# Kernel tuning notes

Hardware: AMD Instinct MI355X
Metric: run time of the kernel (lower is better)

## Reference

```python
import jax, jax.numpy as jnp
import numpy as np

N = 100000      # nodes
E = 1600000     # edges (before self-loops)
F_IN = 128      # dataset.num_features
H1 = 128        # hidden_channels/2
H2 = 256        # hidden_channels
C = 40          # dataset.num_classes
EPS = 1e-5      # BatchNorm eps
NEG_SLOPE = 0.2 # GATConv leaky_relu slope


def setup_inputs() -> dict:
    key = jax.random.key(0)
    ks = jax.random.split(key, 12)
    p = lambda k, shape: jax.random.normal(k, shape, jnp.float32) * 0.1
    x = jax.random.normal(ks[0], (N, F_IN), jnp.float32)
    edge_index = jax.random.randint(ks[1], (2, E), 0, N, dtype=jnp.int64)
    return dict(
        x=x, edge_index=edge_index,
        w1=p(ks[2], (F_IN, H1)), as1=p(ks[3], (H1,)), ad1=p(ks[4], (H1,)), b1=jnp.zeros(H1, jnp.float32),
        g1=jnp.ones(H1, jnp.float32), be1=jnp.zeros(H1, jnp.float32), rm1=jnp.zeros(H1, jnp.float32), rv1=jnp.ones(H1, jnp.float32),
        w2=p(ks[5], (H1, H2)), as2=p(ks[6], (H2,)), ad2=p(ks[7], (H2,)), b2=jnp.zeros(H2, jnp.float32),
        g2=jnp.ones(H2, jnp.float32), be2=jnp.zeros(H2, jnp.float32), rm2=jnp.zeros(H2, jnp.float32), rv2=jnp.ones(H2, jnp.float32),
        w3=p(ks[8], (H2, C)), as3=p(ks[9], (C,)), ad3=p(ks[10], (C,)), b3=jnp.zeros(C, jnp.float32),
    )


def gat_conv(x, src, dst, W, a_src, a_dst, b):
    """PyG GATConv (heads=1, add_self_loops already applied to src/dst)."""
    h = x @ W                                  # [N, F_out]
    alpha_src = h @ a_src                      # [N]
    alpha_dst = h @ a_dst                      # [N]
    logits = jax.nn.leaky_relu(alpha_src[src] + alpha_dst[dst], NEG_SLOPE)  # [E']
    # segment softmax over incoming edges of each dst node
    m = jax.ops.segment_max(logits, dst, num_segments=N)
    e = jnp.exp(logits - m[dst])
    denom = jax.ops.segment_sum(e, dst, num_segments=N)
    alpha = e / denom[dst]                     # [E']
    out = jax.ops.segment_sum(h[src] * alpha[:, None], dst, num_segments=N)
    return out + b


def bn_eval(x, gamma, beta, mean, var):
    return (x - mean) * jax.lax.rsqrt(var + EPS) * gamma + beta


def reference(x, edge_index,
              w1, as1, ad1, b1, g1, be1, rm1, rv1,
              w2, as2, ad2, b2, g2, be2, rm2, rv2,
              w3, as3, ad3, b3):
    # add self-loops once (PyG GATConv default add_self_loops=True)
    loop = jnp.arange(N, dtype=edge_index.dtype)
    src = jnp.concatenate([edge_index[0], loop])
    dst = jnp.concatenate([edge_index[1], loop])
    # eval mode: dropout is identity, BN uses running stats
    h = gat_conv(x, src, dst, w1, as1, ad1, b1)
    h = jnp.tanh(bn_eval(h, g1, be1, rm1, rv1))
    h = gat_conv(h, src, dst, w2, as2, ad2, b2)
    h = jnp.tanh(bn_eval(h, g2, be2, rm2, rv2))
    return gat_conv(h, src, dst, w3, as3, ad3, b3)
```

## Files before the change

kernel.cpp:

```cpp
#include <hip/hip_runtime.h>
#include <hip/hip_bf16.h>
#include <cstddef>

#define N_NODES 100000
#define E_EDGES 1600000
#define TOT_EDGES (E_EDGES + N_NODES)
#define NEG_SLOPE 0.2f
#define BN_EPS 1e-5f
#define NBKT ((N_NODES + 255) / 256)
#define NBA 512

typedef __attribute__((ext_vector_type(8))) short short8;
typedef __attribute__((ext_vector_type(4))) float f32x4;
typedef __attribute__((ext_vector_type(2))) float f32x2;
typedef __attribute__((ext_vector_type(4))) int int32x4;
typedef __attribute__((ext_vector_type(2))) int int32x2;

#if defined(__has_builtin)
#if __has_builtin(__builtin_amdgcn_make_buffer_rsrc) && __has_builtin(__builtin_amdgcn_raw_buffer_load_b128)
#define HAVE_BUFRSRC 1
#endif
#if __has_builtin(__builtin_amdgcn_make_buffer_rsrc) && __has_builtin(__builtin_amdgcn_raw_buffer_load_b64)
#define HAVE_BUF64 1
#endif
#endif

__device__ __forceinline__ unsigned short f2bf(float f) {
    union { float f; unsigned u; } c; c.f = f;
    unsigned u = c.u;
    u += 0x7fffu + ((u >> 16) & 1u);
    return (unsigned short)(u >> 16);
}
__device__ __forceinline__ float bf2f(unsigned short h) {
    union { unsigned u; float f; } c; c.u = ((unsigned)h) << 16;
    return c.f;
}
__device__ __forceinline__ unsigned short f2h(float f) {
    union { _Float16 h; unsigned short u; } c; c.h = (_Float16)f; return c.u;
}
__device__ __forceinline__ float lrelu(float t) {
    return (t > 0.f) ? t : NEG_SLOPE * t;
}
__device__ __forceinline__ float tanh_fast(float x) {
    float e = __expf(2.f * x);
    return 1.f - 2.f / (e + 1.f);
}
__device__ __forceinline__ unsigned short pk_fp8(float a, float b) {
    unsigned v;
    asm volatile("v_cvt_pk_fp8_f32 %0, %1, %2" : "=v"(v) : "v"(a), "v"(b));
    return (unsigned short)v;
}
__device__ __forceinline__ f32x2 unpk_fp8(unsigned u) {
    f32x2 r;
    asm volatile("v_cvt_pk_f32_fp8 %0, %1" : "=v"(r) : "v"(u));
    return r;
}

__device__ __forceinline__ float wave_sum63(float x) {
    x += __int_as_float(__builtin_amdgcn_update_dpp(0, __float_as_int(x), 0x111, 0xf, 0xf, true));
    x += __int_as_float(__builtin_amdgcn_update_dpp(0, __float_as_int(x), 0x112, 0xf, 0xf, true));
    x += __int_as_float(__builtin_amdgcn_update_dpp(0, __float_as_int(x), 0x114, 0xf, 0xf, true));
    x += __int_as_float(__builtin_amdgcn_update_dpp(0, __float_as_int(x), 0x118, 0xf, 0xf, true));
    x += __int_as_float(__builtin_amdgcn_update_dpp(0, __float_as_int(x), 0x142, 0xf, 0xf, true));
    x += __int_as_float(__builtin_amdgcn_update_dpp(0, __float_as_int(x), 0x143, 0xf, 0xf, true));
    return x;
}
__device__ __forceinline__ float wave_sum_bcast(float x) {
    return __int_as_float(__builtin_amdgcn_readlane(__float_as_int(wave_sum63(x)), 63));
}


__global__ __launch_bounds__(256) void csr_hist(const int* __restrict__ ei,
                                                int* __restrict__ bh) {
    __shared__ int h[NBKT];
    int t = threadIdx.x;
    for (int b = t; b < NBKT; b += 256) h[b] = 0;
    __syncthreads();
    int idx = blockIdx.x * 256 + t;
    const int stride = NBA * 256;
    for (int e = idx; e < TOT_EDGES; e += stride) {
        int d = (e < E_EDGES) ? ei[E_EDGES + e] : (e - E_EDGES);
        atomicAdd(&h[((unsigned)d) >> 8], 1);
    }
    __syncthreads();
    for (int b = t; b < NBKT; b += 256) bh[blockIdx.x * NBKT + b] = h[b];
}

__global__ __launch_bounds__(512) void csr_scan_blocks(int* __restrict__ bh,
                                                       int* __restrict__ totals) {
    __shared__ int s[NBA];
    int t = threadIdx.x, bin = blockIdx.x;
    int v = bh[t * NBKT + bin];
    s[t] = v;
    __syncthreads();
    for (int off = 1; off < NBA; off <<= 1) {
        int y = (t >= off) ? s[t - off] : 0;
        __syncthreads();
        s[t] += y;
        __syncthreads();
    }
    bh[t * NBKT + bin] = s[t] - v;
    if (t == NBA - 1) totals[bin] = s[t];
}

__global__ __launch_bounds__(512) void csr_scan_buckets(const int* __restrict__ totals,
                                                        int* __restrict__ starts) {
    __shared__ int s[512];
    int t = threadIdx.x;
    int v = (t < NBKT) ? totals[t] : 0;
    s[t] = v;
    __syncthreads();
    for (int off = 1; off < 512; off <<= 1) {
        int y = (t >= off) ? s[t - off] : 0;
        __syncthreads();
        s[t] += y;
        __syncthreads();
    }
    if (t < NBKT) starts[t] = s[t] - v;
    if (t == 0) starts[NBKT] = TOT_EDGES;
}

__global__ __launch_bounds__(256) void csr_scatter(const int* __restrict__ ei,
                                                   const int* __restrict__ bh,
                                                   const int* __restrict__ starts,
                                                   int* __restrict__ pairs) {
    __shared__ int wp[NBKT];
    int t = threadIdx.x;
    for (int b = t; b < NBKT; b += 256)
        wp[b] = starts[b] + bh[blockIdx.x * NBKT + b];
    __syncthreads();
    int idx = blockIdx.x * 256 + t;
    const int stride = NBA * 256;
    for (int e = idx; e < TOT_EDGES; e += stride) {
        int s, d;
        if (e < E_EDGES) { s = ei[e]; d = ei[E_EDGES + e]; }
        else             { s = e - E_EDGES; d = s; }
        int pos = atomicAdd(&wp[((unsigned)d) >> 8], 1);
        pairs[pos] = s | ((d & 255) << 20);
    }
}

__global__ __launch_bounds__(256) void csr_build(const int* __restrict__ pairs,
                                                 const int* __restrict__ starts,
                                                 int* __restrict__ row_ptr,
                                                 int* __restrict__ src_sorted) {
    __shared__ int nh[256];
    __shared__ int sc[256];
    __shared__ int wp[256];
    int k = blockIdx.x, t = threadIdx.x;
    int bs = starts[k], be = starts[k + 1];
    nh[t] = 0;
    __syncthreads();
    for (int i = bs + t; i < be; i += 256)
        atomicAdd(&nh[((unsigned)pairs[i]) >> 20], 1);
    __syncthreads();
    int v = nh[t];
    sc[t] = v;
    __syncthreads();
    for (int off = 1; off < 256; off <<= 1) {
        int y = (t >= off) ? sc[t - off] : 0;
        __syncthreads();
        sc[t] += y;
        __syncthreads();
    }
    int excl = sc[t] - v;
    int node = k * 256 + t;
    if (node <= N_NODES) row_ptr[node] = bs + excl;
    wp[t] = bs + excl;
    __syncthreads();
    for (int i = bs + t; i < be; i += 256) {
        unsigned p = (unsigned)pairs[i];
        int pos = atomicAdd(&wp[p >> 20], 1);
        src_sorted[pos] = (int)(p & 0xFFFFFu);
    }
}

__global__ __launch_bounds__(256) void wprep_all(
    const float* __restrict__ w1, const float* __restrict__ w2, const float* __restrict__ w3,
    const float* __restrict__ as1, const float* __restrict__ ad1,
    const float* __restrict__ as2, const float* __restrict__ ad2,
    const float* __restrict__ as3, const float* __restrict__ ad3,
    unsigned short* __restrict__ w1th, unsigned short* __restrict__ w1tl,
    unsigned short* __restrict__ w2th, unsigned short* __restrict__ w2tl,
    unsigned short* __restrict__ w3th, unsigned short* __restrict__ w3tl,
    unsigned short* __restrict__ ab1h, unsigned short* __restrict__ ab1l,
    unsigned short* __restrict__ ab3h, unsigned short* __restrict__ ab3l,
    float* __restrict__ ws2f, float* __restrict__ wd2f) {
    const int T1 = 128 * 128, T2 = 256 * 128, T3 = 48 * 256;
    const int W = T1 + T2 + T3;
    int idx = blockIdx.x * 256 + threadIdx.x;
    if (idx < W) {
        float v; unsigned short* th; unsigned short* tl; int o;
        if (idx < T1) {
            int n = idx / 128, k = idx % 128;
            v = w1[k * 128 + n]; th = w1th; tl = w1tl; o = idx;
        } else if (idx < T1 + T2) {
            int i = idx - T1; int n = i / 128, k = i % 128;
            v = w2[k * 256 + n]; th = w2th; tl = w2tl; o = i;
        } else {
            int i = idx - T1 - T2; int n = i / 256, k = i % 256;
            v = (n < 40) ? w3[k * 40 + n] : 0.f; th = w3th; tl = w3tl; o = i;
        }
        unsigned short h = f2bf(v);
        th[o] = h;
        tl[o] = f2bf(v - bf2f(h));
        return;
    }
    int j = idx - W;
    if (j < 2048) {
        int r = j / 128, k = j % 128;
        float v = 0.f;
        if (r < 2) {
            const float* a = r ? ad1 : as1;
            const float* wr = w1 + (size_t)k * 128;
            for (int n = 0; n < 128; n++) v += wr[n] * a[n];
        }
        unsigned short h = f2bf(v);
        ab1h[j] = h; ab1l[j] = f2bf(v - bf2f(h));
    } else if (j < 2048 + 4096) {
        int i = j - 2048; int r = i / 256, k = i % 256;
        float v = 0.f;
        if (r < 2) {
            const float* a = r ? ad3 : as3;
            const float* wr = w3 + (size_t)k * 40;
            for (int n = 0; n < 40; n++) v += wr[n] * a[n];
        }
        unsigned short h = f2bf(v);
        ab3h[i] = h; ab3l[i] = f2bf(v - bf2f(h));
    } else if (j < 2048 + 4096 + 256) {
        int i = j - 2048 - 4096; int r = i / 128, k = i % 128;
        const float* a = r ? ad2 : as2;
        const float* wr = w2 + (size_t)k * 256;
        float v = 0.f;
        for (int n = 0; n < 256; n++) v += wr[n] * a[n];
        if (r == 0) ws2f[k] = v; else wd2f[k] = v;
    }
}

template<int K, int NTILES, int MWAVES, int NWAVES, int NACT, bool ASPLIT, bool ALPHA, bool BNT, bool CFRAG, bool CHALF, bool AF32>
__global__ __launch_bounds__(256) void mfma_gemm(
    const unsigned short* __restrict__ Ahi, const unsigned short* __restrict__ Alo,
    const unsigned short* __restrict__ BThi, const unsigned short* __restrict__ BTlo,
    const unsigned short* __restrict__ ABh, const unsigned short* __restrict__ ABl,
    unsigned short* __restrict__ Chi, int ldc,
    const float* __restrict__ bias, const float* __restrict__ gamma,
    const float* __restrict__ beta, const float* __restrict__ rmean,
    const float* __restrict__ rvar,
    float* __restrict__ asrc, float* __restrict__ adst, int M)
{
    int lane = threadIdx.x & 63;
    int wave = threadIdx.x >> 6;
    int quad = lane >> 4;
    int l16  = lane & 15;
    long mbase = (long)blockIdx.x * (64 * MWAVES) + (long)(wave / NWAVES) * 64;
    int n0 = ((wave % NWAVES) + blockIdx.y * NWAVES) * (NTILES * 16);
    bool aw = ((wave % NWAVES) == 0) && (blockIdx.y == 0);
    const size_t CSTRIDE = (size_t)M * 32;

    size_t roff[4];
#pragma unroll
    for (int i = 0; i < 4; i++) {
        long r = mbase + i * 16 + l16;
        if (r > M - 1) r = M - 1;
        roff[i] = AF32 ? ((size_t)r * K + (size_t)(quad * 8))
                       : ((size_t)r * 32 + (size_t)(quad * 8));
    }
    const unsigned short* bh[NTILES]; const unsigned short* bl[NTILES];
#pragma unroll
    for (int j = 0; j < NTILES; j++) {
        long n = n0 + j * 16 + l16;
        bh[j] = BThi + n * K; bl[j] = BTlo + n * K;
    }
    const unsigned short* bah = nullptr; const unsigned short* bal = nullptr;
    if constexpr (ALPHA) { bah = ABh + (size_t)l16 * K; bal = ABl + (size_t)l16 * K; }
    const int ko = quad * 8;

    f32x4 acc[4][NTILES];
    f32x4 acca[4];
#pragma unroll
    for (int i = 0; i < 4; i++) {
        acca[i] = (f32x4){0.f, 0.f, 0.f, 0.f};
#pragma unroll
        for (int j = 0; j < NTILES; j++)
            acc[i][j] = (f32x4){0.f, 0.f, 0.f, 0.f};
    }

    for (int kc = 0; kc < K / 32; kc++) {
        const int k0 = kc * 32;
        short8 vah[4], vall[4], vbh[NTILES], vbl[NTILES];
#pragma unroll
        for (int i = 0; i < 4; i++) {
            if constexpr (AF32) {
                const float* xf = (const float*)Ahi;
                const float* pa = xf + roff[i] + kc * 32;
                f32x4 va = *(const f32x4*)pa;
                f32x4 vb = *(const f32x4*)(pa + 4);
#pragma unroll
                for (int q = 0; q < 8; q++) {
                    float v = (q < 4) ? va[q] : vb[q - 4];
                    unsigned short h = f2bf(v);
                    vah[i][q] = (short)h;
                    vall[i][q] = (short)f2bf(v - bf2f(h));
                }
            } else {
                const unsigned short* Ah = Ahi + (size_t)kc * CSTRIDE;
                vah[i] = *(const short8*)(Ah + roff[i]);
                if constexpr (ASPLIT) {
                    const unsigned short* Al = Alo + (size_t)kc * CSTRIDE;
                    vall[i] = *(const short8*)(Al + roff[i]);
                }
            }
        }
#pragma unroll
        for (int j = 0; j < NTILES; j++) {
            vbh[j] = *(const short8*)(bh[j] + k0 + ko);
            vbl[j] = *(const short8*)(bl[j] + k0 + ko);
        }
#pragma unroll
        for (int i = 0; i < 4; i++)
#pragma unroll
            for (int j = 0; j < NTILES; j++) {
                acc[i][j] = __builtin_amdgcn_mfma_f32_16x16x32_bf16(vah[i], vbh[j], acc[i][j], 0, 0, 0);
                acc[i][j] = __builtin_amdgcn_mfma_f32_16x16x32_bf16(vah[i], vbl[j], acc[i][j], 0, 0, 0);
                if constexpr (ASPLIT)
                    acc[i][j] = __builtin_amdgcn_mfma_f32_16x16x32_bf16(vall[i], vbh[j], acc[i][j], 0, 0, 0);
            }
        if constexpr (ALPHA) {
            if (aw) {
                short8 vbah = *(const short8*)(bah + k0 + ko);
                short8 vbal = *(const short8*)(bal + k0 + ko);
#pragma unroll
                for (int i = 0; i < 4; i++) {
                    acca[i] = __builtin_amdgcn_mfma_f32_16x16x32_bf16(vah[i], vbah, acca[i], 0, 0, 0);
                    acca[i] = __builtin_amdgcn_mfma_f32_16x16x32_bf16(vah[i], vbal, acca[i], 0, 0, 0);
                    if constexpr (ASPLIT)
                        acca[i] = __builtin_amdgcn_mfma_f32_16x16x32_bf16(vall[i], vbah, acca[i], 0, 0, 0);
                }
            }
        }
    }

#pragma unroll
    for (int i = 0; i < 4; i++)
#pragma unroll
        for (int j = 0; j < NTILES; j++) {
            int col = n0 + j * 16 + l16;
            float bb = 0.f, rs = 1.f, gg = 1.f, bt = 0.f, rm = 0.f;
            if constexpr (BNT) {
                bb = bias[col]; gg = gamma[col]; bt = beta[col];
                rm = rmean[col]; rs = rsqrtf(rvar[col] + BN_EPS);
            }
#pragma unroll
            for (int r = 0; r < 4; r++) {
                long row = mbase + i * 16 + quad * 4 + r;
                if (row < M && col < NACT) {
                    float v = acc[i][j][r];
                    if constexpr (BNT) v = tanh_fast((v + bb - rm) * rs * gg + bt);
                    if constexpr (CFRAG) {
                        Chi[(size_t)(col >> 5) * CSTRIDE + (size_t)row * 32 + (col & 31)] = f2bf(v);
                    } else {
                        Chi[row * ldc + col] = CHALF ? f2h(v) : f2bf(v);
                    }
                }
            }
        }
    if constexpr (ALPHA) {
        if (aw) {
#pragma unroll
            for (int i = 0; i < 4; i++)
#pragma unroll
                for (int r = 0; r < 4; r++) {
                    long row = mbase + i * 16 + quad * 4 + r;
                    if (row < M) {
                        float v = acca[i][r];
                        if (l16 == 0) asrc[row] = v;
                        else if (l16 == 1) adst[row] = v;
                    }
                }
        }
    }
}

__global__ __launch_bounds__(512) void gemm23_fused(
    const unsigned short* __restrict__ Ahi,
    const unsigned short* __restrict__ B2h, const unsigned short* __restrict__ B2l,
    const float* __restrict__ bias, const float* __restrict__ gamma,
    const float* __restrict__ beta, const float* __restrict__ rmean,
    const float* __restrict__ rvar,
    const unsigned short* __restrict__ B3h, const unsigned short* __restrict__ B3l,
    const unsigned short* __restrict__ AB3h, const unsigned short* __restrict__ AB3l,
    unsigned short* __restrict__ h3,
    float* __restrict__ asrc, float* __restrict__ adst, int M)
{
    constexpr int LW = 40;
    __shared__ unsigned short o2l[8 * 64 * LW];

    int lane = threadIdx.x & 63;
    int wave = threadIdx.x >> 6;
    int quad = lane >> 4;
    int l16  = lane & 15;
    long mbase = (long)blockIdx.x * 64;
    const size_t CSTRIDE = (size_t)M * 32;
    const int ko = quad * 8;

    size_t roff[4];
#pragma unroll
    for (int i = 0; i < 4; i++) {
        long r = mbase + i * 16 + l16;
        if (r > M - 1) r = M - 1;
        roff[i] = (size_t)r * 32 + (size_t)ko;
    }
    int n0 = wave * 32;
    const unsigned short* bh[2]; const unsigned short* bl[2];
#pragma unroll
    for (int j = 0; j < 2; j++) {
        long n = n0 + j * 16 + l16;
        bh[j] = B2h + n * 128; bl[j] = B2l + n * 128;
    }

    f32x4 acc[4][2];
#pragma unroll
    for (int i = 0; i < 4; i++)
#pragma unroll
        for (int j = 0; j < 2; j++)
            acc[i][j] = (f32x4){0.f, 0.f, 0.f, 0.f};

#pragma unroll
    for (int kc = 0; kc < 4; kc++) {
        const int k0 = kc * 32;
        const unsigned short* Ah = Ahi + (size_t)kc * CSTRIDE;
        short8 vah[4], vbh[2], vbl[2];
#pragma unroll
        for (int i = 0; i < 4; i++) vah[i] = *(const short8*)(Ah + roff[i]);
#pragma unroll
        for (int j = 0; j < 2; j++) {
            vbh[j] = *(const short8*)(bh[j] + k0 + ko);
            vbl[j] = *(const short8*)(bl[j] + k0 + ko);
        }
#pragma unroll
        for (int i = 0; i < 4; i++)
#pragma unroll
            for (int j = 0; j < 2; j++) {
                acc[i][j] = __builtin_amdgcn_mfma_f32_16x16x32_bf16(vah[i], vbh[j], acc[i][j], 0, 0, 0);
                acc[i][j] = __builtin_amdgcn_mfma_f32_16x16x32_bf16(vah[i], vbl[j], acc[i][j], 0, 0, 0);
            }
    }

#pragma unroll
    for (int j = 0; j < 2; j++) {
        int col = n0 + j * 16 + l16;
        float bb = bias[col], gg = gamma[col], bt = beta[col];
        float rm = rmean[col], rs = rsqrtf(rvar[col] + BN_EPS);
        int cbase = (col >> 5) * 64 * LW + (col & 31);
#pragma unroll
        for (int i = 0; i < 4; i++)
#pragma unroll
            for (int r = 0; r < 4; r++) {
                int li = i * 16 + quad * 4 + r;
                float v = tanh_fast((acc[i][j][r] + bb - rm) * rs * gg + bt);
                o2l[cbase + li * LW] = f2bf(v);
            }
    }
    __syncthreads();

    int rh   = wave >> 2;
    int task = wave & 3;
    int lrow0 = rh * 32 + l16;
    int lrow1 = rh * 32 + 16 + l16;

    const unsigned short* p3h;
    const unsigned short* p3l;
    if (task < 3) {
        p3h = B3h + (size_t)(task * 16 + l16) * 256;
        p3l = B3l + (size_t)(task * 16 + l16) * 256;
    } else {
        p3h = AB3h + (size_t)l16 * 256;
        p3l = AB3l + (size_t)l16 * 256;
    }

    f32x4 a3[2];
    a3[0] = (f32x4){0.f, 0.f, 0.f, 0.f};
    a3[1] = (f32x4){0.f, 0.f, 0.f, 0.f};

#pragma unroll 2
    for (int kc = 0; kc < 8; kc++) {
        const int k0 = kc * 32;
        short8 a0 = *(const short8*)(o2l + (kc * 64 + lrow0) * LW + ko);
        short8 a1 = *(const short8*)(o2l + (kc * 64 + lrow1) * LW + ko);
        short8 vh = *(const short8*)(p3h + k0 + ko);
        short8 vl = *(const short8*)(p3l + k0 + ko);
        a3[0] = __builtin_amdgcn_mfma_f32_16x16x32_bf16(a0, vh, a3[0], 0, 0, 0);
        a3[0] = __builtin_amdgcn_mfma_f32_16x16x32_bf16(a0, vl, a3[0], 0, 0, 0);
        a3[1] = __builtin_amdgcn_mfma_f32_16x16x32_bf16(a1, vh, a3[1], 0, 0, 0);
        a3[1] = __builtin_amdgcn_mfma_f32_16x16x32_bf16(a1, vl, a3[1], 0, 0, 0);
    }

    if (task < 3) {
        int col = task * 16 + l16;
#pragma unroll
        for (int i = 0; i < 2; i++)
#pragma unroll
            for (int r = 0; r < 4; r++) {
                long row = mbase + rh * 32 + i * 16 + quad * 4 + r;
                if (row < M) h3[(size_t)row * 64 + col] = f2h(a3[i][r]);
            }
    } else {
#pragma unroll
        for (int i = 0; i < 2; i++)
#pragma unroll
            for (int r = 0; r < 4; r++) {
                long row = mbase + rh * 32 + i * 16 + quad * 4 + r;
                if (row < M) {
                    if (l16 == 0) asrc[row] = a3[i][r];
                    else if (l16 == 1) adst[row] = a3[i][r];
                }
            }
    }
}

template<int MODE>
__global__ __launch_bounds__(256) void gat_agg_wide(
    const unsigned short* __restrict__ hsrc,
    const float* __restrict__ asrc, const float* __restrict__ adst,
    const int* __restrict__ row_ptr, const int* __restrict__ src_sorted,
    const float* __restrict__ bias, const float* __restrict__ gamma,
    const float* __restrict__ beta, const float* __restrict__ rmean,
    const float* __restrict__ rvar,
    const float* __restrict__ wsn, const float* __restrict__ wdn,
    unsigned short* __restrict__ ohi,
    float* __restrict__ outf,
    float* __restrict__ asrc_n, float* __restrict__ adst_n)
{
    constexpr int SH  = (MODE == 0) ? 8 : 7;
    constexpr int BPL = (MODE == 0) ? 16 : 8;
    constexpr int NF  = (MODE == 2) ? 4 : 8;

    __shared__ __align__(16) float2 esw[4][64];
    __shared__ __align__(16) float red[4][4][132];

    int wave = threadIdx.x >> 6;
    int lane = threadIdx.x & 63;
    int node = blockIdx.x * 4 + wave;
    if (node >= N_NODES) return;

    int start = row_ptr[node];
    int end = row_ptr[node + 1];
    int deg = end - start;
    float ad = adst[node];
    int sub = lane >> 4;
    int foff = (lane & 15) * BPL;
    int tpos = (lane & 3) * 16 + (lane >> 2);

#if defined(HAVE_BUFRSRC) && defined(HAVE_BUF64)
    auto rsrc = __builtin_amdgcn_make_buffer_rsrc((void*)hsrc, (short)0,
                                                  N_NODES << SH, 0x00020000);
#endif

    float acc[NF];
#pragma unroll
    for (int i = 0; i < NF; i++) acc[i] = 0.f;

    auto ld = [&](int vo) {
        if constexpr (MODE == 0) {
#if defined(HAVE_BUFRSRC) && defined(HAVE_BUF64)
            return __builtin_amdgcn_raw_buffer_load_b128(rsrc, vo, 0, 0);
#else
            return *reinterpret_cast<const int32x4*>(
                reinterpret_cast<const char*>(hsrc) + (unsigned)vo);
#endif
        } else {
#if defined(HAVE_BUFRSRC) && defined(HAVE_BUF64)
            return __builtin_amdgcn_raw_buffer_load_b64(rsrc, vo, 0, 0);
#else
            return *reinterpret_cast<const int32x2*>(
                reinterpret_cast<const char*>(hsrc) + (unsigned)vo);
#endif
        }
    };
    auto fmaN = [&](auto u, float ww) {
        if constexpr (MODE == 0) {
            union { decltype(u) v; unsigned w[4]; } c; c.v = u;
#pragma unroll
            for (int i = 0; i < 4; i++) {
                union { unsigned u; _Float16 h[2]; } t; t.u = c.w[i];
                acc[2 * i]     += ww * (float)t.h[0];
                acc[2 * i + 1] += ww * (float)t.h[1];
            }
        } else if constexpr (MODE == 1) {
            union { decltype(u) v; unsigned w[2]; } c; c.v = u;
#pragma unroll
            for (int i = 0; i < 2; i++) {
                f32x2 lo = unpk_fp8(c.w[i]);
                f32x2 hi = unpk_fp8(c.w[i] >> 16);
                acc[4 * i]     += ww * lo.x;
                acc[4 * i + 1] += ww * lo.y;
                acc[4 * i + 2] += ww * hi.x;
                acc[4 * i + 3] += ww * hi.y;
            }
        } else {
            union { decltype(u) v; unsigned w[2]; } c; c.v = u;
#pragma unroll
            for (int i = 0; i < 2; i++) {
                union { unsigned u; _Float16 h[2]; } t; t.u = c.w[i];
                acc[2 * i]     += ww * (float)t.h[0];
                acc[2 * i + 1] += ww * (float)t.h[1];
            }
        }
    };
    auto gather = [&](int nst) {
        const float2* ep = &esw[wave][sub * 16];
#pragma unroll
        for (int b = 0; b < 4; b++) {
            int s0 = b * 4;
            if (s0 < nst) {
                f32x4 p01 = *(const f32x4*)(ep + s0);
                f32x4 p23 = *(const f32x4*)(ep + s0 + 2);
                bool g1 = s0 + 1 < nst, g2 = s0 + 2 < nst, g3 = s0 + 3 < nst;
                auto u0 = ld(__float_as_int(p01.x) + foff);
                decltype(u0) u1, u2, u3;
                if (g1) u1 = ld(__float_as_int(p01.z) + foff);
                if (g2) u2 = ld(__float_as_int(p23.x) + foff);
                if (g3) u3 = ld(__float_as_int(p23.z) + foff);
                fmaN(u0, p01.y);
                if (g1) fmaN(u1, p01.w);
                if (g2) fmaN(u2, p23.y);
                if (g3) fmaN(u3, p23.w);
            }
        }
    };

    if (deg <= 64) {
        int e = start + lane;
        int s = 0; float w = 0.f;
        if (e < end) { s = src_sorted[e]; w = __expf(lrelu(asrc[s] + ad)); }
        float dsum = wave_sum_bcast(w);
        esw[wave][tpos] = make_float2(__int_as_float(s << SH), w * (1.0f / dsum));
        gather((deg + 3) >> 2);
    } else {
        float part = 0.f;
        for (int cs = start; cs < end; cs += 64) {
            int e = cs + lane;
            if (e < end) part += __expf(lrelu(asrc[src_sorted[e]] + ad));
        }
        float inv = 1.0f / wave_sum_bcast(part);
        for (int cs = start; cs < end; cs += 64) {
            int e = cs + lane;
            int s = 0; float w = 0.f;
            if (e < end) { s = src_sorted[e]; w = __expf(lrelu(asrc[s] + ad)) * inv; }
            esw[wave][tpos] = make_float2(__int_as_float(s << SH), w);
            gather((min(64, end - cs) + 3) >> 2);
        }
    }

    if constexpr (MODE == 2) {
        *reinterpret_cast<f32x4*>(&red[wave][sub][(lane & 15) * 4]) =
            (f32x4){acc[0], acc[1], acc[2], acc[3]};
        float t = 0.f;
#pragma unroll
        for (int g = 0; g < 4; g++) t += red[wave][g][lane];
        if (lane < 40) outf[(size_t)node * 40 + lane] = t + bias[lane];
    } else {
        f32x4* dst = reinterpret_cast<f32x4*>(&red[wave][sub][(lane & 15) * 8]);
        dst[0] = (f32x4){acc[0], acc[1], acc[2], acc[3]};
        dst[1] = (f32x4){acc[4], acc[5], acc[6], acc[7]};
        f32x2 tsum = (f32x2){0.f, 0.f};
#pragma unroll
        for (int g = 0; g < 4; g++)
            tsum += *reinterpret_cast<const f32x2*>(&red[wave][g][lane * 2]);

        if constexpr (MODE == 0) {
            float vals[2];
#pragma unroll
            for (int v = 0; v < 2; v++) {
                int f = lane * 2 + v;
                float val = tsum[v] + bias[f];
                float rs = rsqrtf(rvar[f] + BN_EPS);
                vals[v] = tanh_fast((val - rmean[f]) * rs * gamma[f] + beta[f]);
            }
            ohi[(size_t)node * 64 + lane] = pk_fp8(vals[0], vals[1]);
            float ps = vals[0] * wsn[lane * 2] + vals[1] * wsn[lane * 2 + 1];
            float pd = vals[0] * wdn[lane * 2] + vals[1] * wdn[lane * 2 + 1];
            ps = wave_sum63(ps);
            pd = wave_sum63(pd);
            if (lane == 63) { asrc_n[node] = ps; adst_n[node] = pd; }
        } else {
            const size_t CSTRIDE = (size_t)N_NODES * 32;
            unsigned w0 = (unsigned)f2bf(tsum[0]) | ((unsigned)f2bf(tsum[1]) << 16);
            size_t a = (size_t)(lane >> 4) * CSTRIDE + (size_t)node * 32 + ((lane * 2) & 31);
            *reinterpret_cast<unsigned*>(ohi + a) = w0;
        }
    }
}


static inline size_t align256(size_t x) { return (x + 255) & ~(size_t)255; }

extern "C" void kernel_launch(void* const* d_in, const int* in_sizes, int n_in,
                              void* d_out, int out_size, void* d_ws, size_t ws_size,
                              hipStream_t stream) {
    const float* x   = (const float*)d_in[0];
    const int* ei    = (const int*)d_in[1];
    const float* w1  = (const float*)d_in[2];
    const float* as1 = (const float*)d_in[3];
    const float* ad1 = (const float*)d_in[4];
    const float* b1  = (const float*)d_in[5];
    const float* g1  = (const float*)d_in[6];
    const float* be1 = (const float*)d_in[7];
    const float* rm1 = (const float*)d_in[8];
    const float* rv1 = (const float*)d_in[9];
    const float* w2  = (const float*)d_in[10];
    const float* as2 = (const float*)d_in[11];
    const float* ad2 = (const float*)d_in[12];
    const float* b2  = (const float*)d_in[13];
    const float* g2  = (const float*)d_in[14];
    const float* be2 = (const float*)d_in[15];
    const float* rm2 = (const float*)d_in[16];
    const float* rv2 = (const float*)d_in[17];
    const float* w3  = (const float*)d_in[18];
    const float* as3 = (const float*)d_in[19];
    const float* ad3 = (const float*)d_in[20];
    const float* b3  = (const float*)d_in[21];
    float* out = (float*)d_out;

    const size_t P128 = align256((size_t)N_NODES * 128 * 2);
    const size_t P256 = align256((size_t)N_NODES * 256 * 2);

    char* p = (char*)d_ws;
    char* regA = p; p += P256;
    char* regB = p; p += P256;
    unsigned short* o1p  = (unsigned short*)regA;
    unsigned short* h3h  = (unsigned short*)regA;
    unsigned short* h1h  = (unsigned short*)regB;
    unsigned short* g2hi = (unsigned short*)regB;
    int* pairs  = (int*)regB;
    int* bhist  = (int*)(regB + align256((size_t)TOT_EDGES * 4));
    int* totals = (int*)((char*)bhist + align256((size_t)NBA * NBKT * 4));
    int* starts = (int*)((char*)totals + align256((size_t)NBKT * 4));

    float* asrcA = (float*)p; p += align256((size_t)N_NODES * 4);
    float* adstA = (float*)p; p += align256((size_t)N_NODES * 4);
    float* asrcB = (float*)p; p += align256((size_t)N_NODES * 4);
    float* adstB = (float*)p; p += align256((size_t)N_NODES * 4);
    int* row_ptr   = (int*)p; p += align256((size_t)(N_NODES + 1) * 4);
    int* src_sorted = (int*)p; p += align256((size_t)TOT_EDGES * 4);
    unsigned short* w1th = (unsigned short*)p; p += align256(128 * 128 * 2);
    unsigned short* w1tl = (unsigned short*)p; p += align256(128 * 128 * 2);
    unsigned short* w2th = (unsigned short*)p; p += align256(256 * 128 * 2);
    unsigned short* w2tl = (unsigned short*)p; p += align256(256 * 128 * 2);
    unsigned short* w3th = (unsigned short*)p; p += align256(48 * 256 * 2);
    unsigned short* w3tl = (unsigned short*)p; p += align256(48 * 256 * 2);
    unsigned short* ab1h = (unsigned short*)p; p += align256(16 * 128 * 2);
    unsigned short* ab1l = (unsigned short*)p; p += align256(16 * 128 * 2);
    unsigned short* ab3h = (unsigned short*)p; p += align256(16 * 256 * 2);
    unsigned short* ab3l = (unsigned short*)p; p += align256(16 * 256 * 2);
    float* ws2f = (float*)p; p += align256(128 * 4);
    float* wd2f = (float*)p; p += align256(128 * 4);

    const int WTOT = 128 * 128 + 256 * 128 + 48 * 256 + 2048 + 4096 + 256;

    wprep_all<<<(WTOT + 255) / 256, 256, 0, stream>>>(
        w1, w2, w3, as1, ad1, as2, ad2, as3, ad3,
        w1th, w1tl, w2th, w2tl, w3th, w3tl,
        ab1h, ab1l, ab3h, ab3l, ws2f, wd2f);

    csr_hist<<<NBA, 256, 0, stream>>>(ei, bhist);
    csr_scan_blocks<<<NBKT, 512, 0, stream>>>(bhist, totals);
    csr_scan_buckets<<<1, 512, 0, stream>>>(totals, starts);
    csr_scatter<<<NBA, 256, 0, stream>>>(ei, bhist, starts, pairs);
    csr_build<<<NBKT, 256, 0, stream>>>(pairs, starts, row_ptr, src_sorted);

    const int NWB = (N_NODES + 3) / 4;
    const int G64 = (N_NODES + 63) / 64;

    mfma_gemm<128, 2, 1, 4, 128, true, true, false, false, true, true><<<G64, 256, 0, stream>>>(
        (const unsigned short*)x, nullptr, w1th, w1tl, ab1h, ab1l, h1h, 128,
        nullptr, nullptr, nullptr, nullptr, nullptr, asrcA, adstA, N_NODES);
    gat_agg_wide<0><<<NWB, 256, 0, stream>>>(
        h1h, asrcA, adstA, row_ptr, src_sorted,
        b1, g1, be1, rm1, rv1, ws2f, wd2f,
        o1p, nullptr, asrcB, adstB);

    gat_agg_wide<1><<<NWB, 256, 0, stream>>>(
        o1p, asrcB, adstB, row_ptr, src_sorted,
        nullptr, nullptr, nullptr, nullptr, nullptr, nullptr, nullptr,
        g2hi, nullptr, nullptr, nullptr);

    gemm23_fused<<<G64, 512, 0, stream>>>(
        g2hi, w2th, w2tl, b2, g2, be2, rm2, rv2,
        w3th, w3tl, ab3h, ab3l, h3h, asrcA, adstA, N_NODES);

    gat_agg_wide<2><<<NWB, 256, 0, stream>>>(
        h3h, asrcA, adstA, row_ptr, src_sorted,
        b3, nullptr, nullptr, nullptr, nullptr, nullptr, nullptr,
        nullptr, out, nullptr, nullptr);
}
```

Before: 440.6 us.

## Precompute BN2 scale/shift, swizzle blocks across XCDs, split layer-3 MFMA accumulators

Folds the layer-2 bias and eval-mode BatchNorm into a per-column scale and shift, computed once in the weight-prep kernel, so the fused GEMM epilogue does one multiply-add before tanh. Remaps block indices so each XCD handles a contiguous chunk of rows, both in the fused layer-2/3 GEMM and in the second aggregation kernel, aiming for better L2 locality. The layer-3 MFMA loop is fully unrolled and uses two alternating accumulators to break the dependency chain, summing them at the end. The swizzle only helps if neighbouring nodes share sources, and the extra accumulators add register pressure.

New measurement: 443.6 us. About the same (+0.7%).

```diff
diff --git a/kernel.cpp b/kernel.cpp
--- a/kernel.cpp
+++ b/kernel.cpp
@@ -54,6 +54,11 @@
     f32x2 r;
     asm volatile("v_cvt_pk_f32_fp8 %0, %1" : "=v"(r) : "v"(u));
     return r;
+}
+
+__device__ __forceinline__ int xcd_chunk_swz(int b, int nwg) {
+    int q = nwg >> 3, r = nwg & 7, xb = b & 7, ib = b >> 3;
+    return (xb < r ? xb * (q + 1) : r * (q + 1) + (xb - r) * q) + ib;
 }
 
 __device__ __forceinline__ float wave_sum63(float x) {
@@ -180,12 +185,16 @@
     const float* __restrict__ as1, const float* __restrict__ ad1,
     const float* __restrict__ as2, const float* __restrict__ ad2,
     const float* __restrict__ as3, const float* __restrict__ ad3,
+    const float* __restrict__ b2a, const float* __restrict__ g2a,
+    const float* __restrict__ be2a, const float* __restrict__ rm2a,
+    const float* __restrict__ rv2a,
     unsigned short* __restrict__ w1th, unsigned short* __restrict__ w1tl,
     unsigned short* __restrict__ w2th, unsigned short* __restrict__ w2tl,
     unsigned short* __restrict__ w3th, unsigned short* __restrict__ w3tl,
     unsigned short* __restrict__ ab1h, unsigned short* __restrict__ ab1l,
     unsigned short* __restrict__ ab3h, unsigned short* __restrict__ ab3l,
-    float* __restrict__ ws2f, float* __restrict__ wd2f) {
+    float* __restrict__ ws2f, float* __restrict__ wd2f,
+    float* __restrict__ bn2S, float* __restrict__ bn2T) {
     const int T1 = 128 * 128, T2 = 256 * 128, T3 = 48 * 256;
     const int W = T1 + T2 + T3;
     int idx = blockIdx.x * 256 + threadIdx.x;
@@ -234,6 +243,11 @@
         float v = 0.f;
         for (int n = 0; n < 256; n++) v += wr[n] * a[n];
         if (r == 0) ws2f[k] = v; else wd2f[k] = v;
+    } else if (j < 2048 + 4096 + 256 + 256) {
+        int i = j - 2048 - 4096 - 256;
+        float S = rsqrtf(rv2a[i] + BN_EPS) * g2a[i];
+        bn2S[i] = S;
+        bn2T[i] = (b2a[i] - rm2a[i]) * S + be2a[i];
     }
 }
 
@@ -384,9 +398,7 @@
 __global__ __launch_bounds__(512) void gemm23_fused(
     const unsigned short* __restrict__ Ahi,
     const unsigned short* __restrict__ B2h, const unsigned short* __restrict__ B2l,
-    const float* __restrict__ bias, const float* __restrict__ gamma,
-    const float* __restrict__ beta, const float* __restrict__ rmean,
-    const float* __restrict__ rvar,
+    const float* __restrict__ bnS, const float* __restrict__ bnT,
     const unsigned short* __restrict__ B3h, const unsigned short* __restrict__ B3l,
     const unsigned short* __restrict__ AB3h, const unsigned short* __restrict__ AB3l,
     unsigned short* __restrict__ h3,
@@ -399,7 +411,8 @@
     int wave = threadIdx.x >> 6;
     int quad = lane >> 4;
     int l16  = lane & 15;
-    long mbase = (long)blockIdx.x * 64;
+    int g = xcd_chunk_swz(blockIdx.x, gridDim.x);
+    long mbase = (long)g * 64;
     const size_t CSTRIDE = (size_t)M * 32;
     const int ko = quad * 8;
 
@@ -449,16 +462,14 @@
 #pragma unroll
     for (int j = 0; j < 2; j++) {
         int col = n0 + j * 16 + l16;
-        float bb = bias[col], gg = gamma[col], bt = beta[col];
-        float rm = rmean[col], rs = rsqrtf(rvar[col] + BN_EPS);
+        float S = bnS[col], T = bnT[col];
         int cbase = (col >> 5) * 64 * LW + (col & 31);
 #pragma unroll
         for (int i = 0; i < 4; i++)
 #pragma unroll
             for (int r = 0; r < 4; r++) {
                 int li = i * 16 + quad * 4 + r;
-                float v = tanh_fast((acc[i][j][r] + bb - rm) * rs * gg + bt);
-                o2l[cbase + li * LW] = f2bf(v);
+                o2l[cbase + li * LW] = f2bf(tanh_fast(acc[i][j][r] * S + T));
             }
     }
     __syncthreads();
@@ -478,22 +489,29 @@
         p3l = AB3l + (size_t)l16 * 256;
     }
 
-    f32x4 a3[2];
-    a3[0] = (f32x4){0.f, 0.f, 0.f, 0.f};
-    a3[1] = (f32x4){0.f, 0.f, 0.f, 0.f};
-
-#pragma unroll 2
+    f32x4 a3[2][2];
+#pragma unroll
+    for (int i = 0; i < 2; i++)
+#pragma unroll
+        for (int pp = 0; pp < 2; pp++)
+            a3[i][pp] = (f32x4){0.f, 0.f, 0.f, 0.f};
+
+#pragma unroll
     for (int kc = 0; kc < 8; kc++) {
         const int k0 = kc * 32;
+        const int par = kc & 1;
         short8 a0 = *(const short8*)(o2l + (kc * 64 + lrow0) * LW + ko);
         short8 a1 = *(const short8*)(o2l + (kc * 64 + lrow1) * LW + ko);
         short8 vh = *(const short8*)(p3h + k0 + ko);
         short8 vl = *(const short8*)(p3l + k0 + ko);
-        a3[0] = __builtin_amdgcn_mfma_f32_16x16x32_bf16(a0, vh, a3[0], 0, 0, 0);
-        a3[0] = __builtin_amdgcn_mfma_f32_16x16x32_bf16(a0, vl, a3[0], 0, 0, 0);
-        a3[1] = __builtin_amdgcn_mfma_f32_16x16x32_bf16(a1, vh, a3[1], 0, 0, 0);
-        a3[1] = __builtin_amdgcn_mfma_f32_16x16x32_bf16(a1, vl, a3[1], 0, 0, 0);
-    }
+        a3[0][par] = __builtin_amdgcn_mfma_f32_16x16x32_bf16(a0, vh, a3[0][par], 0, 0, 0);
+        a3[0][par] = __builtin_amdgcn_mfma_f32_16x16x32_bf16(a0, vl, a3[0][par], 0, 0, 0);
+        a3[1][par] = __builtin_amdgcn_mfma_f32_16x16x32_bf16(a1, vh, a3[1][par], 0, 0, 0);
+        a3[1][par] = __builtin_amdgcn_mfma_f32_16x16x32_bf16(a1, vl, a3[1][par], 0, 0, 0);
+    }
+    f32x4 r3[2];
+    r3[0] = a3[0][0] + a3[0][1];
+    r3[1] = a3[1][0] + a3[1][1];
 
     if (task < 3) {
         int col = task * 16 + l16;
@@ -502,7 +520,7 @@
 #pragma unroll
             for (int r = 0; r < 4; r++) {
                 long row = mbase + rh * 32 + i * 16 + quad * 4 + r;
-                if (row < M) h3[(size_t)row * 64 + col] = f2h(a3[i][r]);
+                if (row < M) h3[(size_t)row * 64 + col] = f2h(r3[i][r]);
             }
     } else {
 #pragma unroll
@@ -511,14 +529,14 @@
             for (int r = 0; r < 4; r++) {
                 long row = mbase + rh * 32 + i * 16 + quad * 4 + r;
                 if (row < M) {
-                    if (l16 == 0) asrc[row] = a3[i][r];
-                    else if (l16 == 1) adst[row] = a3[i][r];
+                    if (l16 == 0) asrc[row] = r3[i][r];
+                    else if (l16 == 1) adst[row] = r3[i][r];
                 }
             }
     }
 }
 
-template<int MODE>
+template<int MODE, int SWZ>
 __global__ __launch_bounds__(256) void gat_agg_wide(
     const unsigned short* __restrict__ hsrc,
     const float* __restrict__ asrc, const float* __restrict__ adst,
@@ -540,7 +558,9 @@
 
     int wave = threadIdx.x >> 6;
     int lane = threadIdx.x & 63;
-    int node = blockIdx.x * 4 + wave;
+    int bId = blockIdx.x;
+    if constexpr (SWZ) bId = xcd_chunk_swz(bId, gridDim.x);
+    int node = bId * 4 + wave;
     if (node >= N_NODES) return;
 
     int start = row_ptr[node];
@@ -755,13 +775,16 @@
     unsigned short* ab3l = (unsigned short*)p; p += align256(16 * 256 * 2);
     float* ws2f = (float*)p; p += align256(128 * 4);
     float* wd2f = (float*)p; p += align256(128 * 4);
-
-    const int WTOT = 128 * 128 + 256 * 128 + 48 * 256 + 2048 + 4096 + 256;
+    float* bn2S = (float*)p; p += align256(256 * 4);
+    float* bn2T = (float*)p; p += align256(256 * 4);
+
+    const int WTOT = 128 * 128 + 256 * 128 + 48 * 256 + 2048 + 4096 + 256 + 256;
 
     wprep_all<<<(WTOT + 255) / 256, 256, 0, stream>>>(
         w1, w2, w3, as1, ad1, as2, ad2, as3, ad3,
+        b2, g2, be2, rm2, rv2,
         w1th, w1tl, w2th, w2tl, w3th, w3tl,
-        ab1h, ab1l, ab3h, ab3l, ws2f, wd2f);
+        ab1h, ab1l, ab3h, ab3l, ws2f, wd2f, bn2S, bn2T);
 
     csr_hist<<<NBA, 256, 0, stream>>>(ei, bhist);
     csr_scan_blocks<<<NBKT, 512, 0, stream>>>(bhist, totals);
@@ -775,21 +798,21 @@
     mfma_gemm<128, 2, 1, 4, 128, true, true, false, false, true, true><<<G64, 256, 0, stream>>>(
         (const unsigned short*)x, nullptr, w1th, w1tl, ab1h, ab1l, h1h, 128,
         nullptr, nullptr, nullptr, nullptr, nullptr, asrcA, adstA, N_NODES);
-    gat_agg_wide<0><<<NWB, 256, 0, stream>>>(
+    gat_agg_wide<0, 0><<<NWB, 256, 0, stream>>>(
         h1h, asrcA, adstA, row_ptr, src_sorted,
         b1, g1, be1, rm1, rv1, ws2f, wd2f,
         o1p, nullptr, asrcB, adstB);
 
-    gat_agg_wide<1><<<NWB, 256, 0, stream>>>(
+    gat_agg_wide<1, 1><<<NWB, 256, 0, stream>>>(
         o1p, asrcB, adstB, row_ptr, src_sorted,
         nullptr, nullptr, nullptr, nullptr, nullptr, nullptr, nullptr,
         g2hi, nullptr, nullptr, nullptr);
 
     gemm23_fused<<<G64, 512, 0, stream>>>(
-        g2hi, w2th, w2tl, b2, g2, be2, rm2, rv2,
+        g2hi, w2th, w2tl, bn2S, bn2T,
         w3th, w3tl, ab3h, ab3l, h3h, asrcA, adstA, N_NODES);
 
-    gat_agg_wide<2><<<NWB, 256, 0, stream>>>(
+    gat_agg_wide<2, 0><<<NWB, 256, 0, stream>>>(
         h3h, asrcA, adstA, row_ptr, src_sorted,
         b3, nullptr, nullptr, nullptr, nullptr, nullptr, nullptr,
         nullptr, out, nullptr, nullptr);
```
